# Optimization experiments

Hardware: AMD Instinct MI355X
Metric: run time of the kernel (lower is better)

The kernel has to match this reference:

```python
import jax, jax.numpy as jnp
import numpy as np

B, F, E, V = 8192, 16, 32, 100000
D, H1, H2 = 8, 1024, 512
IN = F * E  # 512
EPS = 1e-5


def _bn(x, gamma, beta):
    # x: [D, B, H]; training-mode BatchNorm1d per domain over batch axis (biased var)
    mean = jnp.mean(x, axis=1, keepdims=True)
    var = jnp.mean((x - mean) ** 2, axis=1, keepdims=True)
    return (x - mean) * jax.lax.rsqrt(var + EPS) * gamma[:, None, :] + beta[:, None, :]


def setup_inputs() -> dict:
    key = jax.random.key(0)
    ks = jax.random.split(key, 12)
    feat_ids = jax.random.randint(ks[0], (B, F), 0, V)
    domain_id = jax.random.randint(ks[1], (B,), 0, D)
    emb_tables = jax.random.normal(ks[2], (F, V, E), jnp.float32) * 0.02
    s1 = 1.0 / np.sqrt(IN)
    s2 = 1.0 / np.sqrt(H1)
    s3 = 1.0 / np.sqrt(H2)
    return {
        "feat_ids": feat_ids,
        "domain_id": domain_id,
        "emb_tables": emb_tables,
        "W1": jax.random.uniform(ks[3], (D, H1, IN), jnp.float32, -s1, s1),
        "b1": jax.random.uniform(ks[4], (D, H1), jnp.float32, -s1, s1),
        "g1": jnp.ones((D, H1), jnp.float32),
        "be1": jnp.zeros((D, H1), jnp.float32),
        "W2": jax.random.uniform(ks[5], (D, H2, H1), jnp.float32, -s2, s2),
        "b2": jax.random.uniform(ks[6], (D, H2), jnp.float32, -s2, s2),
        "g2": jnp.ones((D, H2), jnp.float32),
        "be2": jnp.zeros((D, H2), jnp.float32),
        "W3": jax.random.uniform(ks[7], (D, H2), jnp.float32, -s3, s3),
        "b3": jax.random.uniform(ks[8], (D,), jnp.float32, -s3, s3),
    }


def reference(feat_ids, domain_id, emb_tables, W1, b1, g1, be1, W2, b2, g2, be2, W3, b3):
    # embedding lookup per feature then concat -> [B, F*E]
    emb = jax.vmap(lambda tab, ids: tab[ids], in_axes=(0, 1), out_axes=1)(emb_tables, feat_ids)
    emb = emb.reshape(B, IN)
    # all-domain redundant MLP (as in original torch code)
    h = jnp.einsum('bf,dhf->dbh', emb, W1) + b1[:, None, :]          # [D,B,H1]
    h = jax.nn.relu(_bn(h, g1, be1))
    h = jnp.einsum('dbh,dkh->dbk', h, W2) + b2[:, None, :]           # [D,B,H2]
    h = jax.nn.relu(_bn(h, g2, be2))
    out = jax.nn.sigmoid(jnp.einsum('dbk,dk->db', h, W3) + b3[:, None])  # [D,B]
    # mask-select the row matching each sample's domain
    final = jnp.take_along_axis(out.T, domain_id[:, None], axis=1)[:, 0]  # [B]
    return final
```

## Files before the change

kernel.cpp:

```cpp
#include <hip/hip_runtime.h>
#include <hip/hip_bf16.h>

#define B_SZ   8192
#define F_CNT  16
#define E_DIM  32
#define V_CNT  100000
#define D_CNT  8
#define H1     1024
#define H2     512
#define IN_DIM 512
#define EPS_BN 1e-5f

typedef __attribute__((ext_vector_type(8))) unsigned short ushort8;
typedef __attribute__((ext_vector_type(8))) short          frag_ab;
typedef __attribute__((ext_vector_type(4))) float          frag_cd;
typedef __attribute__((ext_vector_type(4))) float          float4v;

__device__ inline unsigned short f2b(float f) {
    unsigned int u = __builtin_bit_cast(unsigned int, f);
    unsigned int r = u + 0x7FFFu + ((u >> 16) & 1u);
    return (unsigned short)(r >> 16);
}
__device__ inline float b2f(unsigned short b) {
    return __builtin_bit_cast(float, (unsigned int)b << 16);
}

__device__ inline void ld_lds16(const unsigned short* g, unsigned short* l) {
    __builtin_amdgcn_global_load_lds(
        (const __attribute__((address_space(1))) unsigned int*)g,
        (__attribute__((address_space(3))) unsigned int*)l, 16, 0, 0);
}

__global__ void k_init(const float* __restrict__ W1, const float* __restrict__ W2,
                       const float* __restrict__ W3, const float* __restrict__ b3,
                       unsigned short* __restrict__ W1c, unsigned short* __restrict__ W2c,
                       unsigned short* __restrict__ W3c, unsigned short* __restrict__ b3c,
                       float* __restrict__ zb) {
    int bid = blockIdx.x, t = threadIdx.x;
    if (bid < 8192) {
        const float* src = (bid < 4096) ? W1 : W2;
        unsigned short* dst = (bid < 4096) ? W1c : W2c;
        long i = ((long)(bid & 4095) * 256 + t) * 4;
        float4v v = *(const float4v*)(src + i);
        dst[i]     = f2b(v[0]);
        dst[i + 1] = f2b(v[1]);
        dst[i + 2] = f2b(v[2]);
        dst[i + 3] = f2b(v[3]);
    } else if (bid == 8192) {
        const float* s = W3 + t * 16;
        unsigned short* d = W3c + t * 16;
#pragma unroll
        for (int j = 0; j < 4; j++) {
            float4v v = *(const float4v*)(s + j * 4);
            d[j * 4 + 0] = f2b(v[0]); d[j * 4 + 1] = f2b(v[1]);
            d[j * 4 + 2] = f2b(v[2]); d[j * 4 + 3] = f2b(v[3]);
        }
        if (t < D_CNT) b3c[t] = f2b(b3[t]);
    } else {
        int i = (bid - 8193) * 1024 + t * 4;
        if (i < 24576) *(float4v*)(zb + i) = (float4v){0.f, 0.f, 0.f, 0.f};
    }
}

__global__ void k_gather(const int* __restrict__ feat_ids,
                         const float* __restrict__ tables,
                         unsigned short* __restrict__ emb) {
    int tid = blockIdx.x * 256 + threadIdx.x;
    int b = tid >> 6;
    int c = tid & 63;
    int f = c >> 2;
    int id = feat_ids[b * F_CNT + f];
    const float* s = tables + ((long)f * V_CNT + id) * E_DIM + (c & 3) * 8;
    float4v v0 = *(const float4v*)s;
    float4v v1 = *(const float4v*)(s + 4);
    ushort8 o;
#pragma unroll
    for (int i = 0; i < 4; i++) { o[i] = f2b(v0[i]); o[i + 4] = f2b(v1[i]); }
    *(ushort8*)(emb + (long)b * IN_DIM + c * 8) = o;
}

__device__ inline void gemm_epilogue(frag_cd acc[4][4],
                                     unsigned short* __restrict__ Cd,
                                     float* __restrict__ gsum, float* __restrict__ gsq,
                                     int N, int d, int m0, int n0,
                                     int wm, int wn, int q, int lr, int lane) {
    float s[4], q2[4];
#pragma unroll
    for (int j = 0; j < 4; j++) { s[j] = 0.f; q2[j] = 0.f; }
#pragma unroll
    for (int i = 0; i < 4; i++) {
        int row = m0 + wm + i * 16 + q * 4;
#pragma unroll
        for (int j = 0; j < 4; j++) {
            int col = n0 + wn + j * 16 + lr;
#pragma unroll
            for (int r = 0; r < 4; r++) {
                float v = acc[i][j][r];
                Cd[(long)(row + r) * N + col] = f2b(v);
                s[j] += v; q2[j] += v * v;
            }
        }
    }
#pragma unroll
    for (int j = 0; j < 4; j++) {
        s[j]  += __shfl_xor(s[j], 16, 64);  s[j]  += __shfl_xor(s[j], 32, 64);
        q2[j] += __shfl_xor(q2[j], 16, 64); q2[j] += __shfl_xor(q2[j], 32, 64);
    }
    if (lane < 16) {
        float* gs = gsum + (long)d * N + n0 + wn;
        float* gq = gsq  + (long)d * N + n0 + wn;
#pragma unroll
        for (int j = 0; j < 4; j++) {
            atomicAdd(&gs[j * 16 + lane], s[j]);
            atomicAdd(&gq[j * 16 + lane], q2[j]);
        }
    }
}

__global__ __launch_bounds__(256, 2)
void k_gemm1(const unsigned short* __restrict__ A,
             const unsigned short* __restrict__ W,
             unsigned short* __restrict__ C,
             float* __restrict__ gsum, float* __restrict__ gsq,
             int M, int N, int K, long aBatchStride, int d0) {
    const int z  = blockIdx.z;
    const int m0 = blockIdx.x * 128;
    const int n0 = blockIdx.y * 128;
    const unsigned short* Ad = A + (long)z * aBatchStride;
    const unsigned short* Wd = W + (long)(d0 + z) * N * K;

    __shared__ unsigned short As[128 * 32];
    __shared__ unsigned short Bs[128 * 32];

    const int t    = threadIdx.x;
    const int wave = t >> 6;
    const int lane = t & 63;
    const int wm   = (wave & 1) << 6;
    const int wn   = (wave >> 1) << 6;
    const int q    = lane >> 4;
    const int lr   = lane & 15;

    const int srow = lane >> 2;
    const int scol = (lane & 3) * 8;
    const unsigned short* aG0 = Ad + (long)(m0 + wave * 32 + srow) * K + scol;
    const unsigned short* aG1 = aG0 + 16 * (long)K;
    const unsigned short* wG0 = Wd + (long)(n0 + wave * 32 + srow) * K + scol;
    const unsigned short* wG1 = wG0 + 16 * (long)K;
    unsigned short* aL0 = &As[(wave * 32) * 32];
    unsigned short* aL1 = &As[(wave * 32 + 16) * 32];
    unsigned short* wL0 = &Bs[(wave * 32) * 32];
    unsigned short* wL1 = &Bs[(wave * 32 + 16) * 32];

    frag_cd acc[4][4];
#pragma unroll
    for (int i = 0; i < 4; i++)
#pragma unroll
        for (int j = 0; j < 4; j++)
            acc[i][j] = (frag_cd){0.f, 0.f, 0.f, 0.f};

    for (int k0 = 0; k0 < K; k0 += 32) {
        ld_lds16(aG0 + k0, aL0);
        ld_lds16(aG1 + k0, aL1);
        ld_lds16(wG0 + k0, wL0);
        ld_lds16(wG1 + k0, wL1);
        __syncthreads();

        frag_ab af[4], bf[4];
#pragma unroll
        for (int i = 0; i < 4; i++) {
            af[i] = *(const frag_ab*)&As[(wm + i * 16 + lr) * 32 + q * 8];
            bf[i] = *(const frag_ab*)&Bs[(wn + i * 16 + lr) * 32 + q * 8];
        }
#pragma unroll
        for (int i = 0; i < 4; i++)
#pragma unroll
            for (int j = 0; j < 4; j++)
                acc[i][j] = __builtin_amdgcn_mfma_f32_16x16x32_bf16(af[i], bf[j], acc[i][j], 0, 0, 0);
        __syncthreads();
    }

    unsigned short* Cd = C + (long)z * M * N;
    gemm_epilogue(acc, Cd, gsum, gsq, N, d0 + z, m0, n0, wm, wn, q, lr, lane);
}

__global__ __launch_bounds__(256, 2)
void k_gemm2(const unsigned short* __restrict__ A,
             const unsigned short* __restrict__ W,
             unsigned short* __restrict__ C,
             float* __restrict__ gsum, float* __restrict__ gsq,
             const float* __restrict__ sc1, const float* __restrict__ sh1,
             int M, int N, int K, long aBatchStride, int d0) {
    const int z  = blockIdx.z;
    const int m0 = blockIdx.x * 128;
    const int n0 = blockIdx.y * 128;
    const unsigned short* Ad = A + (long)z * aBatchStride;
    const unsigned short* Wd = W + (long)(d0 + z) * N * K;

    __shared__ unsigned short As[128 * 32];
    __shared__ unsigned short Bs[128 * 32];

    const int t    = threadIdx.x;
    const int wave = t >> 6;
    const int lane = t & 63;
    const int wm   = (wave & 1) << 6;
    const int wn   = (wave >> 1) << 6;
    const int q    = lane >> 4;
    const int lr   = lane & 15;

    const int srow = lane >> 2;
    const int scol = (lane & 3) * 8;
    const unsigned short* aP0 = Ad + (long)(m0 + wave * 32 + srow) * K + scol;
    const unsigned short* aP1 = aP0 + 16 * (long)K;
    const float* scD = sc1 + (long)(d0 + z) * K;
    const float* shD = sh1 + (long)(d0 + z) * K;
    const unsigned short* wG0 = Wd + (long)(n0 + wave * 32 + srow) * K + scol;
    const unsigned short* wG1 = wG0 + 16 * (long)K;
    unsigned short* aL0w = &As[(wave * 32 + srow) * 32 + scol];
    unsigned short* aL1w = aL0w + 16 * 32;
    unsigned short* wL0 = &Bs[(wave * 32) * 32];
    unsigned short* wL1 = &Bs[(wave * 32 + 16) * 32];

    frag_cd acc[4][4];
#pragma unroll
    for (int i = 0; i < 4; i++)
#pragma unroll
        for (int j = 0; j < 4; j++)
            acc[i][j] = (frag_cd){0.f, 0.f, 0.f, 0.f};

    ushort8 x0 = *(const ushort8*)aP0;
    ushort8 x1 = *(const ushort8*)aP1;

    for (int k0 = 0; k0 < K; k0 += 32) {
        ld_lds16(wG0 + k0, wL0);
        ld_lds16(wG1 + k0, wL1);
        float4v sa = *(const float4v*)(scD + k0 + scol);
        float4v sb = *(const float4v*)(scD + k0 + scol + 4);
        float4v ha = *(const float4v*)(shD + k0 + scol);
        float4v hb = *(const float4v*)(shD + k0 + scol + 4);
        ushort8 y0, y1;
#pragma unroll
        for (int i2 = 0; i2 < 8; i2++) {
            float scv = (i2 < 4) ? sa[i2] : sb[i2 - 4];
            float shv = (i2 < 4) ? ha[i2] : hb[i2 - 4];
            y0[i2] = f2b(fmaxf(b2f(x0[i2]) * scv + shv, 0.f));
            y1[i2] = f2b(fmaxf(b2f(x1[i2]) * scv + shv, 0.f));
        }
        *(ushort8*)aL0w = y0;
        *(ushort8*)aL1w = y1;
        __syncthreads();

        if (k0 + 32 < K) {
            x0 = *(const ushort8*)(aP0 + k0 + 32);
            x1 = *(const ushort8*)(aP1 + k0 + 32);
        }

        frag_ab af[4], bf[4];
#pragma unroll
        for (int i = 0; i < 4; i++) {
            af[i] = *(const frag_ab*)&As[(wm + i * 16 + lr) * 32 + q * 8];
            bf[i] = *(const frag_ab*)&Bs[(wn + i * 16 + lr) * 32 + q * 8];
        }
#pragma unroll
        for (int i = 0; i < 4; i++)
#pragma unroll
            for (int j = 0; j < 4; j++)
                acc[i][j] = __builtin_amdgcn_mfma_f32_16x16x32_bf16(af[i], bf[j], acc[i][j], 0, 0, 0);
        __syncthreads();
    }

    unsigned short* Cd = C + (long)z * M * N;
    gemm_epilogue(acc, Cd, gsum, gsq, N, d0 + z, m0, n0, wm, wn, q, lr, lane);
}

__global__ void k_finalize(const float* __restrict__ gsum, const float* __restrict__ gsq,
                           const float* __restrict__ g, const float* __restrict__ be,
                           float* __restrict__ scale, float* __restrict__ shift, int n,
                           int gOff) {
    int i = blockIdx.x * 256 + threadIdx.x;
    if (i >= n) return;
    float mean = gsum[i] * (1.0f / B_SZ);
    float var  = gsq[i] * (1.0f / B_SZ) - mean * mean;
    float sc   = g[gOff + i] * rsqrtf(var + EPS_BN);
    scale[i] = sc;
    shift[i] = be[gOff + i] - mean * sc;
}

__global__ void k_final(const unsigned short* __restrict__ h2c,
                        const int* __restrict__ domain_id,
                        const float* __restrict__ scale2, const float* __restrict__ shift2,
                        const unsigned short* __restrict__ W3, const unsigned short* __restrict__ b3,
                        float* __restrict__ out, int d0, int nc) {
    int wave = threadIdx.x >> 6, lane = threadIdx.x & 63;
    int b = blockIdx.x * 4 + wave;
    int d = domain_id[b];
    if (d < d0 || d >= d0 + nc) return;
    int o = d * H2 + lane * 8;
    ushort8 v = *(const ushort8*)(h2c + ((long)(d - d0) * B_SZ + b) * H2 + lane * 8);
    ushort8 w = *(const ushort8*)(W3 + o);
    float sum = 0.f;
#pragma unroll
    for (int i = 0; i < 8; i++) {
        float x = b2f(v[i]) * scale2[o + i] + shift2[o + i];
        sum += fmaxf(x, 0.f) * b2f(w[i]);
    }
#pragma unroll
    for (int off = 32; off > 0; off >>= 1) sum += __shfl_xor(sum, off, 64);
    if (lane == 0)
        out[b] = 1.f / (1.f + expf(-(sum + b2f(b3[d]))));
}

__global__ void k_sentinel(float* __restrict__ out, int n) {
    int i = blockIdx.x * 256 + threadIdx.x;
    if (i < n) out[i] = 0.25f;
}

extern "C" void kernel_launch(void* const* d_in, const int* in_sizes, int n_in,
                              void* d_out, int out_size, void* d_ws, size_t ws_size,
                              hipStream_t stream) {
    const int*   feat_ids  = (const int*)d_in[0];
    const int*   domain_id = (const int*)d_in[1];
    const float* tables = (const float*)d_in[2];
    const float* W1  = (const float*)d_in[3];
    const float* g1  = (const float*)d_in[5];
    const float* be1 = (const float*)d_in[6];
    const float* W2  = (const float*)d_in[7];
    const float* g2  = (const float*)d_in[9];
    const float* be2 = (const float*)d_in[10];
    const float* W3  = (const float*)d_in[11];
    const float* b3  = (const float*)d_in[12];

    char* ws = (char*)d_ws;
    float* gsum1  = (float*)ws;
    float* gsq1   = gsum1 + 8192;
    float* gsum2  = gsq1 + 8192;
    float* gsq2   = gsum2 + 4096;
    float* scale1 = gsq2 + 4096;
    float* shift1 = scale1 + 8192;
    float* scale2 = shift1 + 8192;
    float* shift2 = scale2 + 4096;
    unsigned short* W1c = (unsigned short*)(ws + (1L  << 20));
    unsigned short* W2c = (unsigned short*)(ws + (9L  << 20));
    unsigned short* W3c = (unsigned short*)(ws + (17L << 20));
    unsigned short* b3c = W3c + D_CNT * H2;
    unsigned short* emb = (unsigned short*)(ws + (18L << 20));

    const long h1Elems = (long)B_SZ * H1;
    const long h2Elems = (long)B_SZ * H2;
    const long perDom  = (h1Elems + h2Elems) * 2;
    const long baseOff = 26L << 20;
    int NC = 0;
    for (int cand = 8; cand >= 1; cand >>= 1)
        if (baseOff + (long)cand * perDom <= (long)ws_size) { NC = cand; break; }
    if (NC == 0) {
        k_sentinel<<<dim3((out_size + 255) / 256), dim3(256), 0, stream>>>(
            (float*)d_out, out_size);
        return;
    }
    unsigned short* h1c = (unsigned short*)(ws + baseOff);
    unsigned short* h2c = h1c + (long)NC * h1Elems;

    k_init<<<dim3(8217), dim3(256), 0, stream>>>(W1, W2, W3, b3, W1c, W2c, W3c, b3c, gsum1);
    k_gather<<<dim3(2048), dim3(256), 0, stream>>>(feat_ids, tables, emb);

    for (int d0 = 0; d0 < D_CNT; d0 += NC) {
        k_gemm1<<<dim3(64, 8, NC), dim3(256), 0, stream>>>(
            emb, W1c, h1c, gsum1, gsq1, 8192, 1024, 512, 0L, d0);
        k_finalize<<<dim3(NC * 4), dim3(256), 0, stream>>>(
            gsum1 + d0 * H1, gsq1 + d0 * H1, g1, be1,
            scale1 + d0 * H1, shift1 + d0 * H1, NC * H1, d0 * H1);
        k_gemm2<<<dim3(64, 4, NC), dim3(256), 0, stream>>>(
            h1c, W2c, h2c, gsum2, gsq2, scale1, shift1, 8192, 512, 1024, h1Elems, d0);
        k_finalize<<<dim3(NC * 2), dim3(256), 0, stream>>>(
            gsum2 + d0 * H2, gsq2 + d0 * H2, g2, be2,
            scale2 + d0 * H2, shift2 + d0 * H2, NC * H2, d0 * H2);
        k_final<<<dim3(2048), dim3(256), 0, stream>>>(
            h2c, domain_id, scale2, shift2, W3c, b3c, (float*)d_out, d0, NC);
    }
}
```

Before: 491.7 us.

## Rewrite first GEMM with 256x256 tiles and double-buffered LDS prefetch

Replaces the 128x128, 256-thread first-layer GEMM with a 256x256 tile, 512-thread kernel. It double-buffers LDS over a 64-wide K step and issues the next tile's global-to-LDS loads while the current sub-tile feeds the MFMAs. It uses explicit waitcnt/barrier scheduling and s_setprio around the MFMA bursts. The aim is to raise operand reuse per LDS load and hide global-load latency. In exchange, LDS use grows to about 128KB per block, which limits occupancy to one block per CU and makes correctness depend on the hand-tuned waitcnt counts.

```diff
diff --git a/kernel.cpp b/kernel.cpp
--- a/kernel.cpp
+++ b/kernel.cpp
@@ -79,6 +79,130 @@
     *(ushort8*)(emb + (long)b * IN_DIM + c * 8) = o;
 }
 
+__global__ __launch_bounds__(512, 2)
+void k_gemm1(const unsigned short* __restrict__ A,
+             const unsigned short* __restrict__ W,
+             unsigned short* __restrict__ C,
+             float* __restrict__ gsum, float* __restrict__ gsq,
+             int M, int N, int K, long aBatchStride, int d0) {
+    const int z  = blockIdx.z;
+    const int m0 = blockIdx.x * 256;
+    const int n0 = blockIdx.y * 256;
+    const unsigned short* Ad = A + (long)z * aBatchStride;
+    const unsigned short* Wd = W + (long)(d0 + z) * (long)N * K;
+
+    __shared__ unsigned short As[2 * 2 * 8192];
+    __shared__ unsigned short Bs[2 * 2 * 8192];
+
+    const int t    = threadIdx.x;
+    const int w    = t >> 6;
+    const int lane = t & 63;
+    const int wr   = w >> 2;
+    const int wc   = w & 3;
+    const int q    = lane >> 4;
+    const int lr   = lane & 15;
+
+    const int srow = lane >> 2;
+    const int scol = (lane & 3) * 8;
+    const unsigned short* aGb[2];
+    const unsigned short* wGb[2];
+    aGb[0] = Ad + (long)(m0 + w * 16 + srow) * K + scol;
+    aGb[1] = aGb[0] + (long)128 * K;
+    wGb[0] = Wd + (long)(n0 + w * 16 + srow) * K + scol;
+    wGb[1] = wGb[0] + (long)128 * K;
+
+    frag_cd acc[8][4];
+#pragma unroll
+    for (int i = 0; i < 8; i++)
+#pragma unroll
+        for (int j = 0; j < 4; j++)
+            acc[i][j] = (frag_cd){0.f, 0.f, 0.f, 0.f};
+
+    const int NT = K >> 6;
+
+#pragma unroll
+    for (int p = 0; p < 4; ++p) {
+        const int kh = p >> 1, sg = p & 1;
+        ld_lds16(aGb[sg] + kh * 32, &As[kh * 8192 + sg * 4096 + w * 512]);
+        ld_lds16(wGb[sg] + kh * 32, &Bs[kh * 8192 + sg * 4096 + w * 512]);
+    }
+
+    for (int tt = 0; tt < NT; ++tt) {
+        const int b = tt & 1;
+        const bool lastT = (tt == NT - 1);
+#pragma unroll
+        for (int p = 0; p < 4; ++p) {
+            const int ks = p >> 1;
+            const int mh = p & 1;
+            if (p == 0 || p == 2) {
+                if (p == 2 && lastT)
+                    asm volatile("s_waitcnt vmcnt(0)" ::: "memory");
+                else
+                    asm volatile("s_waitcnt vmcnt(4)" ::: "memory");
+                __builtin_amdgcn_s_barrier();
+            }
+            frag_ab af[4], bf[4];
+            const unsigned short* Ap = &As[b * 16384 + ks * 8192];
+            const unsigned short* Bp = &Bs[b * 16384 + ks * 8192];
+#pragma unroll
+            for (int i = 0; i < 4; ++i) {
+                af[i] = *(const frag_ab*)&Ap[(wr * 128 + (mh * 4 + i) * 16 + lr) * 32 + q * 8];
+                bf[i] = *(const frag_ab*)&Bp[(wc * 64 + i * 16 + lr) * 32 + q * 8];
+            }
+            if (!lastT) {
+                const long ko = (long)(tt + 1) * 64 + ks * 32;
+                ld_lds16(aGb[mh] + ko, &As[(b ^ 1) * 16384 + ks * 8192 + mh * 4096 + w * 512]);
+                ld_lds16(wGb[mh] + ko, &Bs[(b ^ 1) * 16384 + ks * 8192 + mh * 4096 + w * 512]);
+            }
+            __builtin_amdgcn_s_barrier();
+            asm volatile("s_waitcnt lgkmcnt(0)" ::: "memory");
+            __builtin_amdgcn_sched_barrier(0);
+            __builtin_amdgcn_s_setprio(1);
+#pragma unroll
+            for (int i = 0; i < 4; ++i)
+#pragma unroll
+                for (int j = 0; j < 4; ++j)
+                    acc[mh * 4 + i][j] = __builtin_amdgcn_mfma_f32_16x16x32_bf16(
+                        af[i], bf[j], acc[mh * 4 + i][j], 0, 0, 0);
+            __builtin_amdgcn_s_setprio(0);
+            __builtin_amdgcn_s_barrier();
+        }
+    }
+
+    unsigned short* Cd = C + (long)z * (long)M * N;
+    float s[4], q2[4];
+#pragma unroll
+    for (int j = 0; j < 4; j++) { s[j] = 0.f; q2[j] = 0.f; }
+#pragma unroll
+    for (int I = 0; I < 8; ++I) {
+        int row = m0 + wr * 128 + I * 16 + q * 4;
+#pragma unroll
+        for (int j = 0; j < 4; ++j) {
+            int col = n0 + wc * 64 + j * 16 + lr;
+#pragma unroll
+            for (int r = 0; r < 4; ++r) {
+                float v = acc[I][j][r];
+                Cd[(long)(row + r) * N + col] = f2b(v);
+                s[j] += v; q2[j] += v * v;
+            }
+        }
+    }
+#pragma unroll
+    for (int j = 0; j < 4; j++) {
+        s[j]  += __shfl_xor(s[j], 16, 64);  s[j]  += __shfl_xor(s[j], 32, 64);
+        q2[j] += __shfl_xor(q2[j], 16, 64); q2[j] += __shfl_xor(q2[j], 32, 64);
+    }
+    if (lane < 16) {
+        float* gs = gsum + (long)(d0 + z) * N + n0 + wc * 64;
+        float* gq = gsq  + (long)(d0 + z) * N + n0 + wc * 64;
+#pragma unroll
+        for (int j = 0; j < 4; j++) {
+            atomicAdd(&gs[j * 16 + lane], s[j]);
+            atomicAdd(&gq[j * 16 + lane], q2[j]);
+        }
+    }
+}
+
 __device__ inline void gemm_epilogue(frag_cd acc[4][4],
                                      unsigned short* __restrict__ Cd,
                                      float* __restrict__ gsum, float* __restrict__ gsq,
@@ -115,72 +239,6 @@
             atomicAdd(&gq[j * 16 + lane], q2[j]);
         }
     }
-}
-
-__global__ __launch_bounds__(256, 2)
-void k_gemm1(const unsigned short* __restrict__ A,
-             const unsigned short* __restrict__ W,
-             unsigned short* __restrict__ C,
-             float* __restrict__ gsum, float* __restrict__ gsq,
-             int M, int N, int K, long aBatchStride, int d0) {
-    const int z  = blockIdx.z;
-    const int m0 = blockIdx.x * 128;
-    const int n0 = blockIdx.y * 128;
-    const unsigned short* Ad = A + (long)z * aBatchStride;
-    const unsigned short* Wd = W + (long)(d0 + z) * N * K;
-
-    __shared__ unsigned short As[128 * 32];
-    __shared__ unsigned short Bs[128 * 32];
-
-    const int t    = threadIdx.x;
-    const int wave = t >> 6;
-    const int lane = t & 63;
-    const int wm   = (wave & 1) << 6;
-    const int wn   = (wave >> 1) << 6;
-    const int q    = lane >> 4;
-    const int lr   = lane & 15;
-
-    const int srow = lane >> 2;
-    const int scol = (lane & 3) * 8;
-    const unsigned short* aG0 = Ad + (long)(m0 + wave * 32 + srow) * K + scol;
-    const unsigned short* aG1 = aG0 + 16 * (long)K;
-    const unsigned short* wG0 = Wd + (long)(n0 + wave * 32 + srow) * K + scol;
-    const unsigned short* wG1 = wG0 + 16 * (long)K;
-    unsigned short* aL0 = &As[(wave * 32) * 32];
-    unsigned short* aL1 = &As[(wave * 32 + 16) * 32];
-    unsigned short* wL0 = &Bs[(wave * 32) * 32];
-    unsigned short* wL1 = &Bs[(wave * 32 + 16) * 32];
-
-    frag_cd acc[4][4];
-#pragma unroll
-    for (int i = 0; i < 4; i++)
-#pragma unroll
-        for (int j = 0; j < 4; j++)
-            acc[i][j] = (frag_cd){0.f, 0.f, 0.f, 0.f};
-
-    for (int k0 = 0; k0 < K; k0 += 32) {
-        ld_lds16(aG0 + k0, aL0);
-        ld_lds16(aG1 + k0, aL1);
-        ld_lds16(wG0 + k0, wL0);
-        ld_lds16(wG1 + k0, wL1);
-        __syncthreads();
-
-        frag_ab af[4], bf[4];
-#pragma unroll
-        for (int i = 0; i < 4; i++) {
-            af[i] = *(const frag_ab*)&As[(wm + i * 16 + lr) * 32 + q * 8];
-            bf[i] = *(const frag_ab*)&Bs[(wn + i * 16 + lr) * 32 + q * 8];
-        }
-#pragma unroll
-        for (int i = 0; i < 4; i++)
-#pragma unroll
-            for (int j = 0; j < 4; j++)
-                acc[i][j] = __builtin_amdgcn_mfma_f32_16x16x32_bf16(af[i], bf[j], acc[i][j], 0, 0, 0);
-        __syncthreads();
-    }
-
-    unsigned short* Cd = C + (long)z * M * N;
-    gemm_epilogue(acc, Cd, gsum, gsq, N, d0 + z, m0, n0, wm, wn, q, lr, lane);
 }
 
 __global__ __launch_bounds__(256, 2)
@@ -363,7 +421,7 @@
     k_gather<<<dim3(2048), dim3(256), 0, stream>>>(feat_ids, tables, emb);
 
     for (int d0 = 0; d0 < D_CNT; d0 += NC) {
-        k_gemm1<<<dim3(64, 8, NC), dim3(256), 0, stream>>>(
+        k_gemm1<<<dim3(32, 4, NC), dim3(512), 0, stream>>>(
             emb, W1c, h1c, gsum1, gsq1, 8192, 1024, 512, 0L, d0);
         k_finalize<<<dim3(NC * 4), dim3(256), 0, stream>>>(
             gsum1 + d0 * H1, gsq1 + d0 * H1, g1, be1,
```

New measurement: 478.5 us. 1.03x faster.
